# Performance work log

Measured on AMD Instinct MI355X. Metric: run time of the kernel, lower is better.

The kernel has to match this reference:

```python
import jax, jax.numpy as jnp
import numpy as np

N_FEATURES = 100
D_TOKEN = 192
D_HID = D_TOKEN // 2


def setup_inputs() -> dict:
    key = jax.random.key(0)
    k_x, k_w1, k_b1, k_w2, k_b2 = jax.random.split(key, 5)
    # Per-feature stacked weights (equivalent to n_features separate tiny MLPs).
    # Linear(1, h): weight [h, 1] -> stacked as W1 [F, h]; bias b1 [F, h]
    # Linear(h, d): weight [d, h] -> stacked as W2 [F, h, d]; bias b2 [F, d]
    lim1 = 1.0  # kaiming-uniform bound for fan_in=1: sqrt(1/1)
    lim2 = 1.0 / np.sqrt(D_HID)
    x = jax.random.normal(k_x, (4096, N_FEATURES), dtype=jnp.float32)
    W1 = jax.random.uniform(k_w1, (N_FEATURES, D_HID), jnp.float32, -lim1, lim1)
    b1 = jax.random.uniform(k_b1, (N_FEATURES, D_HID), jnp.float32, -lim1, lim1)
    W2 = jax.random.uniform(k_w2, (N_FEATURES, D_HID, D_TOKEN), jnp.float32, -lim2, lim2)
    b2 = jax.random.uniform(k_b2, (N_FEATURES, D_TOKEN), jnp.float32, -lim2, lim2)
    return {"x": x, "W1": W1, "b1": b1, "W2": W2, "b2": b2}


def reference(x, W1, b1, W2, b2):
    # x: [B, F] scalar per feature
    # hidden: [B, F, H] = x[b,f] * W1[f,h] + b1[f,h]
    h = jax.nn.gelu(x[:, :, None] * W1[None, :, :] + b1[None, :, :], approximate=False)
    # out: [B, F, D] = einsum over hidden dim, one small GEMM per feature batched
    out = jnp.einsum('bfh,fhd->bfd', h, W2) + b2[None, :, :]
    return out
```

## Files before the change

kernel.cpp:

```cpp
#include <hip/hip_runtime.h>
#include <hip/hip_bf16.h>

#define N_F 100
#define N_B 4096
#define DH 96
#define DT 192
#define BM 64
#define HPAD 100
#define SPAD 196

#define SYNC_LDS() asm volatile("s_waitcnt lgkmcnt(0)\n\ts_barrier" ::: "memory")

typedef unsigned short u16;
typedef unsigned int u32;
typedef __bf16 bf16x8 __attribute__((ext_vector_type(8)));
typedef float f32x4 __attribute__((ext_vector_type(4)));

union FragAB { bf16x8 v; uint2 q2[2]; uint4 q4; };

static __device__ __forceinline__ u16 f2bf(float v) {
    u32 b = __float_as_uint(v);
    return (u16)((b + 0x7FFFu + ((b >> 16) & 1u)) >> 16);
}

static __device__ __forceinline__ float gelu_fast(float p) {
    float p3 = p * p * p;
    float y  = fmaf(0.044715f, p3, p);
    float t  = exp2f(2.3022083f * y);
    float r  = __builtin_amdgcn_rcpf(1.0f + t);
    return fmaf(-p, r, p);
}

__global__ void convert_w2_kernel(const float* __restrict__ W2, u16* __restrict__ W2F) {
    int idx = blockIdx.x * 256 + threadIdx.x;
    if (idx >= N_F * DH * (DT / 4)) return;
    int f  = idx / (DH * (DT / 4));
    int r  = idx - f * (DH * (DT / 4));
    int k  = r / (DT / 4);
    int d4 = (r - k * (DT / 4)) * 4;
    const float4 w = *(const float4*)&W2[(f * DH + k) * DT + d4];

    int ks = k >> 5;
    int kr = k & 31;
    int q  = (kr >> 2) & 3;
    int e  = ((kr >> 4) << 2) | (kr & 3);
    u16* base = W2F + (size_t)f * (DH * DT);
    int DT16 = d4 >> 4;
    int m    = d4 & 15;
    size_t i0 = ((size_t)(ks * 12 + DT16) * 64 + q * 16 + m) * 8 + e;
    base[i0]      = f2bf(w.x);
    base[i0 + 8]  = f2bf(w.y);
    base[i0 + 16] = f2bf(w.z);
    base[i0 + 24] = f2bf(w.w);
}

template <bool USE_WS>
__global__ __launch_bounds__(256, 4) void mlp_tok_kernel(
    const float* __restrict__ x, const float* __restrict__ W1,
    const float* __restrict__ b1, const float* __restrict__ W2,
    const float* __restrict__ b2, const u16* __restrict__ W2F,
    float* __restrict__ out)
{
    const int f   = blockIdx.x;
    const int b0  = blockIdx.y * BM;
    const int tid = threadIdx.x;
    const int lane = tid & 63;
    const int wv   = tid >> 6;

    __shared__ float x_lds[BM];
    __shared__ u16 h_lds[BM][HPAD];
    __shared__ float stage[32][SPAD];
    __shared__ u16 w2t_lds[USE_WS ? 1 : DT][HPAD];

    if (tid < BM) x_lds[tid] = x[(size_t)(b0 + tid) * N_F + f];
    SYNC_LDS();

    {
        const int row = tid & (BM - 1);
        const int kc  = (tid >> 6) * 24;
        const float xv = x_lds[row];
        #pragma unroll
        for (int c = 0; c < 6; ++c) {
            const int k = kc + c * 4;
            const float4 w1v = *(const float4*)&W1[f * DH + k];
            const float4 b1v = *(const float4*)&b1[f * DH + k];
            float g0 = gelu_fast(fmaf(xv, w1v.x, b1v.x));
            float g1 = gelu_fast(fmaf(xv, w1v.y, b1v.y));
            float g2 = gelu_fast(fmaf(xv, w1v.z, b1v.z));
            float g3 = gelu_fast(fmaf(xv, w1v.w, b1v.w));
            uint2 pk;
            pk.x = (u32)f2bf(g0) | ((u32)f2bf(g1) << 16);
            pk.y = (u32)f2bf(g2) | ((u32)f2bf(g3) << 16);
            *(uint2*)&h_lds[row][k] = pk;
        }
    }

    if constexpr (!USE_WS) {
        #pragma unroll
        for (int i = 0; i < (DT * DH) / (256 * 4); ++i) {
            const int e = (i * 256 + tid) * 4;
            const int k = e / DT;
            const int n = e - k * DT;
            const float4 wv4 = *(const float4*)&W2[(f * DH + k) * DT + n];
            w2t_lds[n + 0][k] = f2bf(wv4.x);
            w2t_lds[n + 1][k] = f2bf(wv4.y);
            w2t_lds[n + 2][k] = f2bf(wv4.z);
            w2t_lds[n + 3][k] = f2bf(wv4.w);
        }
    }
    SYNC_LDS();

    const int q = lane >> 4;
    const int m = lane & 15;

    f32x4 acc[3][4];
    #pragma unroll
    for (int dt = 0; dt < 3; ++dt)
        #pragma unroll
        for (int bt = 0; bt < 4; ++bt)
            acc[dt][bt] = (f32x4){0.f, 0.f, 0.f, 0.f};

    const u16* __restrict__ w2ff = USE_WS ? (W2F + (size_t)f * (DH * DT)) : nullptr;

    #pragma unroll
    for (int ks = 0; ks < 3; ++ks) {
        const int k0 = ks * 32 + q * 4;
        FragAB a[3], hb[4];
        #pragma unroll
        for (int dt = 0; dt < 3; ++dt) {
            if constexpr (USE_WS) {
                a[dt].q4 = *(const uint4*)&w2ff[((ks * 12 + wv * 3 + dt) * 64 + lane) * 8];
            } else {
                const int d = wv * 48 + dt * 16 + m;
                a[dt].q2[0] = *(const uint2*)&w2t_lds[d][k0];
                a[dt].q2[1] = *(const uint2*)&w2t_lds[d][k0 + 16];
            }
        }
        #pragma unroll
        for (int bt = 0; bt < 4; ++bt) {
            hb[bt].q2[0] = *(const uint2*)&h_lds[bt * 16 + m][k0];
            hb[bt].q2[1] = *(const uint2*)&h_lds[bt * 16 + m][k0 + 16];
        }
        #pragma unroll
        for (int dt = 0; dt < 3; ++dt)
            #pragma unroll
            for (int bt = 0; bt < 4; ++bt)
                acc[dt][bt] = __builtin_amdgcn_mfma_f32_16x16x32_bf16(
                    a[dt].v, hb[bt].v, acc[dt][bt], 0, 0, 0);
    }

    const int dbase = wv * 48;
    f32x4 b2q[3];
    #pragma unroll
    for (int dt = 0; dt < 3; ++dt)
        b2q[dt] = *(const f32x4*)&b2[f * DT + dbase + dt * 16 + q * 4];

    #pragma unroll
    for (int hh = 0; hh < 2; ++hh) {
        if (hh) SYNC_LDS();
        #pragma unroll
        for (int bt2 = 0; bt2 < 2; ++bt2) {
            const int bt = hh * 2 + bt2;
            #pragma unroll
            for (int dt = 0; dt < 3; ++dt) {
                f32x4 v = acc[dt][bt] + b2q[dt];
                *(f32x4*)&stage[bt2 * 16 + m][dbase + dt * 16 + q * 4] = v;
            }
        }
        SYNC_LDS();
        #pragma unroll
        for (int i = 0; i < 6; ++i) {
            const int idx = i * 256 + tid;
            const int row = idx / 48;
            const int c4  = idx - row * 48;
            f32x4 v = *(const f32x4*)&stage[row][c4 * 4];
            __builtin_nontemporal_store(
                v, (f32x4*)&out[((size_t)(b0 + hh * 32 + row) * N_F + f) * DT + c4 * 4]);
        }
    }
}

extern "C" void kernel_launch(void* const* d_in, const int* in_sizes, int n_in,
                              void* d_out, int out_size, void* d_ws, size_t ws_size,
                              hipStream_t stream) {
    const float* x  = (const float*)d_in[0];
    const float* W1 = (const float*)d_in[1];
    const float* b1 = (const float*)d_in[2];
    const float* W2 = (const float*)d_in[3];
    const float* b2 = (const float*)d_in[4];
    float* out = (float*)d_out;

    const size_t w2f_bytes = (size_t)N_F * DT * DH * sizeof(u16);
    dim3 grid(N_F, N_B / BM);

    if (ws_size >= w2f_bytes) {
        u16* W2F = (u16*)d_ws;
        convert_w2_kernel<<<(N_F * DH * (DT / 4) + 255) / 256, 256, 0, stream>>>(W2, W2F);
        mlp_tok_kernel<true><<<grid, 256, 0, stream>>>(x, W1, b1, W2, b2, W2F, out);
    } else {
        mlp_tok_kernel<false><<<grid, 256, 0, stream>>>(x, W1, b1, W2, b2, nullptr, out);
    }
}
```

Before: 75.76 us.

## Process four features per block in a loop to cut grid size

```diff
diff --git a/kernel.cpp b/kernel.cpp
--- a/kernel.cpp
+++ b/kernel.cpp
@@ -6,6 +6,7 @@
 #define DH 96
 #define DT 192
 #define BM 64
+#define FCHUNK 4
 #define HPAD 100
 #define SPAD 196
 
@@ -61,121 +62,121 @@
     const float* __restrict__ b2, const u16* __restrict__ W2F,
     float* __restrict__ out)
 {
-    const int f   = blockIdx.x;
+    const int fc0 = blockIdx.x * FCHUNK;
     const int b0  = blockIdx.y * BM;
     const int tid = threadIdx.x;
     const int lane = tid & 63;
     const int wv   = tid >> 6;
 
-    __shared__ float x_lds[BM];
+    __shared__ float x_lds[FCHUNK][BM];
     __shared__ u16 h_lds[BM][HPAD];
     __shared__ float stage[32][SPAD];
-    __shared__ u16 w2t_lds[USE_WS ? 1 : DT][HPAD];
-
-    if (tid < BM) x_lds[tid] = x[(size_t)(b0 + tid) * N_F + f];
-    SYNC_LDS();
-
-    {
-        const int row = tid & (BM - 1);
-        const int kc  = (tid >> 6) * 24;
-        const float xv = x_lds[row];
-        #pragma unroll
-        for (int c = 0; c < 6; ++c) {
-            const int k = kc + c * 4;
-            const float4 w1v = *(const float4*)&W1[f * DH + k];
-            const float4 b1v = *(const float4*)&b1[f * DH + k];
-            float g0 = gelu_fast(fmaf(xv, w1v.x, b1v.x));
-            float g1 = gelu_fast(fmaf(xv, w1v.y, b1v.y));
-            float g2 = gelu_fast(fmaf(xv, w1v.z, b1v.z));
-            float g3 = gelu_fast(fmaf(xv, w1v.w, b1v.w));
-            uint2 pk;
-            pk.x = (u32)f2bf(g0) | ((u32)f2bf(g1) << 16);
-            pk.y = (u32)f2bf(g2) | ((u32)f2bf(g3) << 16);
-            *(uint2*)&h_lds[row][k] = pk;
-        }
-    }
-
-    if constexpr (!USE_WS) {
-        #pragma unroll
-        for (int i = 0; i < (DT * DH) / (256 * 4); ++i) {
-            const int e = (i * 256 + tid) * 4;
-            const int k = e / DT;
-            const int n = e - k * DT;
-            const float4 wv4 = *(const float4*)&W2[(f * DH + k) * DT + n];
-            w2t_lds[n + 0][k] = f2bf(wv4.x);
-            w2t_lds[n + 1][k] = f2bf(wv4.y);
-            w2t_lds[n + 2][k] = f2bf(wv4.z);
-            w2t_lds[n + 3][k] = f2bf(wv4.w);
-        }
+
+    if (tid < BM) {
+        const float4 xi = *(const float4*)&x[(size_t)(b0 + tid) * N_F + fc0];
+        x_lds[0][tid] = xi.x; x_lds[1][tid] = xi.y;
+        x_lds[2][tid] = xi.z; x_lds[3][tid] = xi.w;
     }
     SYNC_LDS();
 
     const int q = lane >> 4;
     const int m = lane & 15;
 
-    f32x4 acc[3][4];
-    #pragma unroll
-    for (int dt = 0; dt < 3; ++dt)
-        #pragma unroll
-        for (int bt = 0; bt < 4; ++bt)
-            acc[dt][bt] = (f32x4){0.f, 0.f, 0.f, 0.f};
-
-    const u16* __restrict__ w2ff = USE_WS ? (W2F + (size_t)f * (DH * DT)) : nullptr;
-
-    #pragma unroll
-    for (int ks = 0; ks < 3; ++ks) {
-        const int k0 = ks * 32 + q * 4;
-        FragAB a[3], hb[4];
-        #pragma unroll
-        for (int dt = 0; dt < 3; ++dt) {
-            if constexpr (USE_WS) {
-                a[dt].q4 = *(const uint4*)&w2ff[((ks * 12 + wv * 3 + dt) * 64 + lane) * 8];
-            } else {
-                const int d = wv * 48 + dt * 16 + m;
-                a[dt].q2[0] = *(const uint2*)&w2t_lds[d][k0];
-                a[dt].q2[1] = *(const uint2*)&w2t_lds[d][k0 + 16];
-            }
-        }
-        #pragma unroll
-        for (int bt = 0; bt < 4; ++bt) {
-            hb[bt].q2[0] = *(const uint2*)&h_lds[bt * 16 + m][k0];
-            hb[bt].q2[1] = *(const uint2*)&h_lds[bt * 16 + m][k0 + 16];
-        }
-        #pragma unroll
-        for (int dt = 0; dt < 3; ++dt)
-            #pragma unroll
-            for (int bt = 0; bt < 4; ++bt)
-                acc[dt][bt] = __builtin_amdgcn_mfma_f32_16x16x32_bf16(
-                    a[dt].v, hb[bt].v, acc[dt][bt], 0, 0, 0);
-    }
-
-    const int dbase = wv * 48;
-    f32x4 b2q[3];
-    #pragma unroll
-    for (int dt = 0; dt < 3; ++dt)
-        b2q[dt] = *(const f32x4*)&b2[f * DT + dbase + dt * 16 + q * 4];
-
-    #pragma unroll
-    for (int hh = 0; hh < 2; ++hh) {
-        if (hh) SYNC_LDS();
-        #pragma unroll
-        for (int bt2 = 0; bt2 < 2; ++bt2) {
-            const int bt = hh * 2 + bt2;
-            #pragma unroll
-            for (int dt = 0; dt < 3; ++dt) {
-                f32x4 v = acc[dt][bt] + b2q[dt];
-                *(f32x4*)&stage[bt2 * 16 + m][dbase + dt * 16 + q * 4] = v;
+    for (int ff = 0; ff < FCHUNK; ++ff) {
+        const int f = fc0 + ff;
+
+        {
+            const int row = tid & (BM - 1);
+            const int kc  = (tid >> 6) * 24;
+            const float xv = x_lds[ff][row];
+            #pragma unroll
+            for (int c = 0; c < 6; ++c) {
+                const int k = kc + c * 4;
+                const float4 w1v = *(const float4*)&W1[f * DH + k];
+                const float4 b1v = *(const float4*)&b1[f * DH + k];
+                float g0 = gelu_fast(fmaf(xv, w1v.x, b1v.x));
+                float g1 = gelu_fast(fmaf(xv, w1v.y, b1v.y));
+                float g2 = gelu_fast(fmaf(xv, w1v.z, b1v.z));
+                float g3 = gelu_fast(fmaf(xv, w1v.w, b1v.w));
+                uint2 pk;
+                pk.x = (u32)f2bf(g0) | ((u32)f2bf(g1) << 16);
+                pk.y = (u32)f2bf(g2) | ((u32)f2bf(g3) << 16);
+                *(uint2*)&h_lds[row][k] = pk;
             }
         }
         SYNC_LDS();
-        #pragma unroll
-        for (int i = 0; i < 6; ++i) {
-            const int idx = i * 256 + tid;
-            const int row = idx / 48;
-            const int c4  = idx - row * 48;
-            f32x4 v = *(const f32x4*)&stage[row][c4 * 4];
-            __builtin_nontemporal_store(
-                v, (f32x4*)&out[((size_t)(b0 + hh * 32 + row) * N_F + f) * DT + c4 * 4]);
+
+        f32x4 acc[3][4];
+        #pragma unroll
+        for (int dt = 0; dt < 3; ++dt)
+            #pragma unroll
+            for (int bt = 0; bt < 4; ++bt)
+                acc[dt][bt] = (f32x4){0.f, 0.f, 0.f, 0.f};
+
+        const u16* __restrict__ w2ff = USE_WS ? (W2F + (size_t)f * (DH * DT)) : nullptr;
+
+        #pragma unroll
+        for (int ks = 0; ks < 3; ++ks) {
+            const int k0 = ks * 32 + q * 4;
+            FragAB a[3], hb[4];
+            #pragma unroll
+            for (int dt = 0; dt < 3; ++dt) {
+                if constexpr (USE_WS) {
+                    a[dt].q4 = *(const uint4*)&w2ff[((ks * 12 + wv * 3 + dt) * 64 + lane) * 8];
+                } else {
+                    const int d = wv * 48 + dt * 16 + m;
+                    u16 tmp[8];
+                    #pragma unroll
+                    for (int e = 0; e < 8; ++e) {
+                        const int k = ks * 32 + (e >> 2) * 16 + q * 4 + (e & 3);
+                        tmp[e] = f2bf(W2[((size_t)f * DH + k) * DT + d]);
+                    }
+                    a[dt].q4 = make_uint4(
+                        (u32)tmp[0] | ((u32)tmp[1] << 16), (u32)tmp[2] | ((u32)tmp[3] << 16),
+                        (u32)tmp[4] | ((u32)tmp[5] << 16), (u32)tmp[6] | ((u32)tmp[7] << 16));
+                }
+            }
+            #pragma unroll
+            for (int bt = 0; bt < 4; ++bt) {
+                hb[bt].q2[0] = *(const uint2*)&h_lds[bt * 16 + m][k0];
+                hb[bt].q2[1] = *(const uint2*)&h_lds[bt * 16 + m][k0 + 16];
+            }
+            #pragma unroll
+            for (int dt = 0; dt < 3; ++dt)
+                #pragma unroll
+                for (int bt = 0; bt < 4; ++bt)
+                    acc[dt][bt] = __builtin_amdgcn_mfma_f32_16x16x32_bf16(
+                        a[dt].v, hb[bt].v, acc[dt][bt], 0, 0, 0);
+        }
+
+        const int dbase = wv * 48;
+        f32x4 b2q[3];
+        #pragma unroll
+        for (int dt = 0; dt < 3; ++dt)
+            b2q[dt] = *(const f32x4*)&b2[f * DT + dbase + dt * 16 + q * 4];
+
+        #pragma unroll
+        for (int hh = 0; hh < 2; ++hh) {
+            SYNC_LDS();
+            #pragma unroll
+            for (int bt2 = 0; bt2 < 2; ++bt2) {
+                const int bt = hh * 2 + bt2;
+                #pragma unroll
+                for (int dt = 0; dt < 3; ++dt) {
+                    f32x4 v = acc[dt][bt] + b2q[dt];
+                    *(f32x4*)&stage[bt2 * 16 + m][dbase + dt * 16 + q * 4] = v;
+                }
+            }
+            SYNC_LDS();
+            #pragma unroll
+            for (int i = 0; i < 6; ++i) {
+                const int idx = i * 256 + tid;
+                const int row = idx / 48;
+                const int c4  = idx - row * 48;
+                f32x4 v = *(const f32x4*)&stage[row][c4 * 4];
+                __builtin_nontemporal_store(
+                    v, (f32x4*)&out[((size_t)(b0 + hh * 32 + row) * N_F + f) * DT + c4 * 4]);
+            }
         }
     }
 }
@@ -191,7 +192,7 @@
     float* out = (float*)d_out;
 
     const size_t w2f_bytes = (size_t)N_F * DT * DH * sizeof(u16);
-    dim3 grid(N_F, N_B / BM);
+    dim3 grid(N_F / FCHUNK, N_B / BM);
 
     if (ws_size >= w2f_bytes) {
         u16* W2F = (u16*)d_ws;
```

New measurement: 99.49 us. 1.31x slower.
